# Kernel tuning notes

Hardware: AMD Instinct MI355X
Metric: run time of the kernel (lower is better)

The kernel has to match this reference:

```python
import jax, jax.numpy as jnp
import numpy as np

HEAD_SIZE = 64
INPUT_SIZE = 1024
B, T = 8, 2048


def setup_inputs() -> dict:
    key = jax.random.key(0)
    kx, kq, kk, kv = jax.random.split(key, 4)
    x = jax.random.normal(kx, (B, T, INPUT_SIZE), dtype=jnp.float32)
    s = 1.0 / np.sqrt(INPUT_SIZE)
    Wq = jax.random.uniform(kq, (INPUT_SIZE, HEAD_SIZE), minval=-s, maxval=s, dtype=jnp.float32)
    Wk = jax.random.uniform(kk, (INPUT_SIZE, HEAD_SIZE), minval=-s, maxval=s, dtype=jnp.float32)
    Wv = jax.random.uniform(kv, (INPUT_SIZE, HEAD_SIZE), minval=-s, maxval=s, dtype=jnp.float32)
    return {"x": x, "Wq": Wq, "Wk": Wk, "Wv": Wv}


def reference(x, Wq, Wk, Wv):
    # Faithful to the torch module: scores = K @ Q^T (note: keys times queries^T),
    # causal mask on upper triangle of that matrix, softmax over last axis,
    # dropout treated as identity (eval), then scores @ V.
    q = jnp.einsum('bti,ih->bth', x, Wq)  # [B,T,H]
    k = jnp.einsum('bti,ih->bth', x, Wk)
    v = jnp.einsum('bti,ih->bth', x, Wv)
    scale = HEAD_SIZE ** -0.5
    scores = jnp.einsum('bth,bsh->bts', k, q) * scale  # [B,T,T] = K Q^T
    Tlen = x.shape[1]
    causal = jnp.tril(jnp.ones((Tlen, Tlen), dtype=bool))
    scores = jnp.where(causal, scores, -jnp.inf)
    w = jax.nn.softmax(scores, axis=-1)
    out = jnp.einsum('bts,bsh->bth', w, v)  # [B,T,H]
    return out
```

## Files before the change

### kernel.cpp

```cpp
#include <hip/hip_runtime.h>

typedef __bf16 bf16_t;
typedef bf16_t bf16x8 __attribute__((ext_vector_type(8)));
typedef float f32x4 __attribute__((ext_vector_type(4)));

#define NB 8
#define TT 2048
#define DIN 1024
#define HH 64
#define MM (NB * TT)

__device__ __forceinline__ unsigned short f2bf(float f) {
    unsigned int u = __float_as_uint(f);
    u += 0x7fffu + ((u >> 16) & 1u);
    return (unsigned short)(u >> 16);
}

__device__ __forceinline__ int block_detect_f32(const unsigned int* __restrict__ xw,
                                                int tid, int* sflag) {
    if (tid < 64) {
        unsigned int u = xw[tid];
        unsigned int e = (u >> 7) & 0xFFu;
        unsigned long long m = __ballot(e >= 100u && e <= 150u);
        if (tid == 0) *sflag = (__popcll(m) < 48) ? 1 : 0;
    }
    __syncthreads();
    return *sflag;
}

__global__ __launch_bounds__(256) void transpose_w_kernel(
    const void* __restrict__ Wq, const void* __restrict__ Wk,
    const void* __restrict__ Wv, const unsigned int* __restrict__ xw,
    unsigned short* __restrict__ Wt) {
    __shared__ int sflag;
    __shared__ unsigned short ts[64][68];
    const int tid = threadIdx.x;
    const int isf32 = block_detect_f32(xw, tid, &sflag);
    const int w = blockIdx.x >> 4, kt = blockIdx.x & 15;
    const void* W = (w == 0) ? Wq : (w == 1) ? Wk : Wv;
    const int kk = tid >> 4, nn = (tid & 15) * 4;
#pragma unroll
    for (int j = 0; j < 4; ++j) {
        int k = kk + j * 16;
        if (isf32) {
            float4 f = *(const float4*)((const float*)W + (size_t)(kt * 64 + k) * 64 + nn);
            ts[k][nn + 0] = f2bf(f.x); ts[k][nn + 1] = f2bf(f.y);
            ts[k][nn + 2] = f2bf(f.z); ts[k][nn + 3] = f2bf(f.w);
        } else {
            *(uint2*)&ts[k][nn] =
                *(const uint2*)((const unsigned short*)W + (size_t)(kt * 64 + k) * 64 + nn);
        }
    }
    __syncthreads();
    const int n = tid >> 2, k0 = (tid & 3) * 16;
    unsigned short tmp[16];
#pragma unroll
    for (int j = 0; j < 16; ++j) tmp[j] = ts[k0 + j][n];
    unsigned short* dst = Wt + (size_t)(w * 64 + n) * 1024 + kt * 64 + k0;
    *(uint4*)(dst + 0) = *(uint4*)&tmp[0];
    *(uint4*)(dst + 8) = *(uint4*)&tmp[8];
}

__global__ __launch_bounds__(256) void proj_kernel(
    const void* __restrict__ xraw, const unsigned short* __restrict__ Wt,
    unsigned short* __restrict__ qbuf, unsigned short* __restrict__ kbuf,
    unsigned short* __restrict__ vtbuf) {
    __shared__ int sflag;
    __shared__ __align__(16) unsigned short xs[32][72];
    __shared__ __align__(16) unsigned short wts[192][72];

    const int tid = threadIdx.x;
    const int isf32 = block_detect_f32((const unsigned int*)xraw, tid, &sflag);
    const int m0 = blockIdx.x * 32;
    const int wave = tid >> 6, lane = tid & 63, quad = lane >> 4, l15 = lane & 15;
    const int rw = wave & 1, cw = wave >> 1;

    f32x4 acc[6];
#pragma unroll
    for (int c = 0; c < 6; ++c) acc[c] = (f32x4){0.f, 0.f, 0.f, 0.f};

    const float* xf = (const float*)xraw;
    const unsigned short* xb = (const unsigned short*)xraw;
    const int xr = tid >> 3, xc = (tid & 7) * 8;

    for (int k0 = 0; k0 < DIN; k0 += 64) {
        if (isf32) {
            const float* gp = xf + (size_t)(m0 + xr) * DIN + k0 + xc;
            float4 f0 = *(const float4*)(gp + 0);
            float4 f1 = *(const float4*)(gp + 4);
            unsigned short t[8] = {f2bf(f0.x), f2bf(f0.y), f2bf(f0.z), f2bf(f0.w),
                                   f2bf(f1.x), f2bf(f1.y), f2bf(f1.z), f2bf(f1.w)};
            *(uint4*)&xs[xr][xc] = *(uint4*)t;
        } else {
            *(uint4*)&xs[xr][xc] =
                *(const uint4*)(xb + (size_t)(m0 + xr) * DIN + k0 + xc);
        }
#pragma unroll
        for (int j = 0; j < 6; ++j) {
            int u = tid + j * 256;
            int n = u >> 3, cc = (u & 7) * 8;
            *(uint4*)&wts[n][cc] = *(const uint4*)(Wt + (size_t)n * 1024 + k0 + cc);
        }
        __syncthreads();
#pragma unroll
        for (int ks = 0; ks < 2; ++ks) {
            bf16x8 a = *(const bf16x8*)&xs[rw * 16 + l15][ks * 32 + quad * 8];
#pragma unroll
            for (int c = 0; c < 6; ++c) {
                bf16x8 bb = *(const bf16x8*)&wts[(cw * 6 + c) * 16 + l15][ks * 32 + quad * 8];
                acc[c] = __builtin_amdgcn_mfma_f32_16x16x32_bf16(a, bb, acc[c], 0, 0, 0);
            }
        }
        __syncthreads();
    }

#pragma unroll
    for (int c = 0; c < 6; ++c) {
        int cg = cw * 6 + c;
        int wsel = cg >> 2;
        int nn = (cg & 3) * 16 + l15;
#pragma unroll
        for (int reg = 0; reg < 4; ++reg) {
            int m = m0 + rw * 16 + quad * 4 + reg;
            unsigned short bv = f2bf(acc[c][reg]);
            if (wsel == 0)      qbuf[(size_t)m * HH + nn] = bv;
            else if (wsel == 1) kbuf[(size_t)m * HH + nn] = bv;
            else {
                int bb = m >> 11, t = m & 2047;
                vtbuf[((size_t)bb * HH + nn) * TT + t] = bv;
            }
        }
    }
}

__global__ __launch_bounds__(256) void attn_kernel(
    const unsigned short* __restrict__ rowbuf,
    const unsigned short* __restrict__ colbuf,
    const unsigned short* __restrict__ vtbuf,
    float* __restrict__ O_part,
    float* __restrict__ l_part) {

    __shared__ __align__(16) unsigned short Qr_s[64][72];
    __shared__ __align__(16) unsigned short Kc_s[64][72];
    __shared__ __align__(16) unsigned short Vt_s[64][72];
    __shared__ __align__(16) unsigned short P_s[4][16][72];

    const int tid  = threadIdx.x;
    const int bx   = blockIdx.x;
    const int b    = blockIdx.y;
    int rt, ch;
    if (bx < 8)       { rt = bx;                 ch = 0; }
    else if (bx < 24) { rt = 8 + ((bx - 8) >> 1);  ch = (bx - 8) & 1; }
    else if (bx < 48) { rt = 16 + (bx - 24) / 3;   ch = (bx - 24) % 3; }
    else              { rt = 24 + ((bx - 48) >> 2); ch = (bx - 48) & 3; }
    const int nct = min(8, rt + 1 - ch * 8);
    const int t0 = rt * 64;
    const int slot = b * 80 + bx;

    const int wave = tid >> 6, lane = tid & 63, quad = lane >> 4, l15 = lane & 15;
    const int sr = tid >> 2, sc = (tid & 3) * 16;

    {
        const uint4* g = (const uint4*)(rowbuf + ((size_t)b * TT + t0 + sr) * HH + sc);
        *(uint4*)&Qr_s[sr][sc + 0] = g[0];
        *(uint4*)&Qr_s[sr][sc + 8] = g[1];
    }

    f32x4 o[4];
#pragma unroll
    for (int c = 0; c < 4; ++c) o[c] = (f32x4){0.f, 0.f, 0.f, 0.f};
    float ls[4] = {0.f, 0.f, 0.f, 0.f};

    const float SCL2 = 0.125f * 1.4426950408889634f;

    for (int i = 0; i < nct; ++i) {
        const int stc = ch * 8 + i;
        const int s0 = stc * 64;
        {
            const uint4* gk = (const uint4*)(colbuf + ((size_t)b * TT + s0 + sr) * HH + sc);
            uint4 k0 = gk[0], k1 = gk[1];
            const uint4* gv = (const uint4*)(vtbuf + ((size_t)b * HH + sr) * TT + s0 + sc);
            uint4 v0 = gv[0], v1 = gv[1];
            *(uint4*)&Kc_s[sr][sc + 0] = k0;
            *(uint4*)&Kc_s[sr][sc + 8] = k1;
            *(uint4*)&Vt_s[sr][sc + 0] = v0;
            *(uint4*)&Vt_s[sr][sc + 8] = v1;
        }
        __syncthreads();

        f32x4 scf[4];
#pragma unroll
        for (int c = 0; c < 4; ++c) scf[c] = (f32x4){0.f, 0.f, 0.f, 0.f};
#pragma unroll
        for (int ks = 0; ks < 2; ++ks) {
            bf16x8 a = *(const bf16x8*)&Qr_s[wave * 16 + l15][ks * 32 + quad * 8];
#pragma unroll
            for (int c = 0; c < 4; ++c) {
                bf16x8 bb = *(const bf16x8*)&Kc_s[c * 16 + l15][ks * 32 + quad * 8];
                scf[c] = __builtin_amdgcn_mfma_f32_16x16x32_bf16(a, bb, scf[c], 0, 0, 0);
            }
        }

        const bool diag = (stc == rt);
#pragma unroll
        for (int r = 0; r < 4; ++r) {
            const int tg = t0 + wave * 16 + quad * 4 + r;
#pragma unroll
            for (int c = 0; c < 4; ++c) {
                float arg = fmaf(scf[c][r], SCL2, -30.f);
                if (diag && (s0 + c * 16 + l15) > tg) arg = -200.f;
                float p = __builtin_amdgcn_exp2f(arg);
                P_s[wave][quad * 4 + r][c * 16 + l15] = f2bf(p);
                ls[r] += p;
            }
        }
#pragma unroll
        for (int ks = 0; ks < 2; ++ks) {
            bf16x8 ap = *(const bf16x8*)&P_s[wave][l15][ks * 32 + quad * 8];
#pragma unroll
            for (int c = 0; c < 4; ++c) {
                bf16x8 bv = *(const bf16x8*)&Vt_s[c * 16 + l15][ks * 32 + quad * 8];
                o[c] = __builtin_amdgcn_mfma_f32_16x16x32_bf16(ap, bv, o[c], 0, 0, 0);
            }
        }
        __syncthreads();
    }

#pragma unroll
    for (int r = 0; r < 4; ++r) {
#pragma unroll
        for (int off = 1; off < 16; off <<= 1) ls[r] += __shfl_xor(ls[r], off);
    }
    if (l15 == 0) {
#pragma unroll
        for (int r = 0; r < 4; ++r)
            l_part[(size_t)slot * 64 + wave * 16 + quad * 4 + r] = ls[r];
    }
#pragma unroll
    for (int c = 0; c < 4; ++c)
#pragma unroll
        for (int r = 0; r < 4; ++r)
            O_part[(size_t)slot * 4096 + (wave * 16 + quad * 4 + r) * 64 + c * 16 + l15] = o[c][r];
}

__global__ __launch_bounds__(256) void combine_kernel(
    const float* __restrict__ O_part, const float* __restrict__ l_part,
    const unsigned int* __restrict__ xw, void* __restrict__ outraw) {
    __shared__ int sflag;
    const int tid = threadIdx.x;
    const int isf32 = block_detect_f32(xw, tid, &sflag);
    const int rt = blockIdx.x, b = blockIdx.y;
    const int nch = rt / 8 + 1;
    const int off = (rt < 8) ? rt : (rt < 16) ? 8 + 2 * (rt - 8)
                   : (rt < 24) ? 24 + 3 * (rt - 16) : 48 + 4 * (rt - 24);
    const int slot0 = b * 80 + off;

    const int row = tid >> 2, cb = (tid & 3) * 16;
    f32x4 a[4];
#pragma unroll
    for (int q = 0; q < 4; ++q) a[q] = (f32x4){0.f, 0.f, 0.f, 0.f};
    float l = 0.f;
    for (int j = 0; j < nch; ++j) {
        const f32x4* p = (const f32x4*)(O_part + (size_t)(slot0 + j) * 4096 + row * 64 + cb);
#pragma unroll
        for (int q = 0; q < 4; ++q) a[q] += p[q];
        l += l_part[(size_t)(slot0 + j) * 64 + row];
    }
    const float inv = 1.f / l;
    const size_t base = ((size_t)b * TT + rt * 64 + row) * HH + cb;
    if (isf32) {
        float* outf = (float*)outraw;
#pragma unroll
        for (int q = 0; q < 4; ++q) {
            f32x4 v = a[q] * inv;
            *(f32x4*)(outf + base + q * 4) = v;
        }
    } else {
        unsigned short h[16];
#pragma unroll
        for (int q = 0; q < 4; ++q)
#pragma unroll
            for (int e = 0; e < 4; ++e) h[q * 4 + e] = f2bf(a[q][e] * inv);
        unsigned short* outb = (unsigned short*)outraw;
        *(uint4*)(outb + base + 0) = *(uint4*)&h[0];
        *(uint4*)(outb + base + 8) = *(uint4*)&h[8];
    }
}

extern "C" void kernel_launch(void* const* d_in, const int* in_sizes, int n_in,
                              void* d_out, int out_size, void* d_ws, size_t ws_size,
                              hipStream_t stream) {
    const void* x  = d_in[0];
    const void* Wq = d_in[1];
    const void* Wk = d_in[2];
    const void* Wv = d_in[3];
    unsigned short* ws = (unsigned short*)d_ws;

    unsigned short* qbuf  = ws;
    unsigned short* kbuf  = ws + (size_t)MM * HH;
    unsigned short* vtbuf = ws + (size_t)2 * MM * HH;
    unsigned short* wtbuf = ws + (size_t)3 * MM * HH;
    float* O_part = (float*)(ws + (size_t)3 * MM * HH + 3 * 65536);
    float* l_part = O_part + (size_t)640 * 4096;

    hipLaunchKernelGGL(transpose_w_kernel, dim3(48), dim3(256), 0, stream,
                       Wq, Wk, Wv, (const unsigned int*)x, wtbuf);
    hipLaunchKernelGGL(proj_kernel, dim3(512), dim3(256), 0, stream,
                       x, wtbuf, qbuf, kbuf, vtbuf);
    hipLaunchKernelGGL(attn_kernel, dim3(80, 8), dim3(256), 0, stream,
                       kbuf, qbuf, vtbuf, O_part, l_part);
    hipLaunchKernelGGL(combine_kernel, dim3(32, 8), dim3(256), 0, stream,
                       O_part, l_part, (const unsigned int*)x, d_out);
}
```

Before: 160.3 us.

## Double the projection row tile and prefetch next K-slice into registers

The projection kernel now processes 64 rows per block instead of 32, giving each wave a 2x6 MFMA tile so each loaded weight fragment is reused across two row tiles, and halves the grid to 256 blocks. Global loads for the next K slice are issued into registers before the current slice's MFMAs, overlapping memory latency with compute. This raises register pressure and halves the number of blocks, which may reduce occupancy and CU coverage on a large-CU device.

```diff
diff --git a/kernel.cpp b/kernel.cpp
--- a/kernel.cpp
+++ b/kernel.cpp
@@ -66,71 +66,112 @@
     unsigned short* __restrict__ qbuf, unsigned short* __restrict__ kbuf,
     unsigned short* __restrict__ vtbuf) {
     __shared__ int sflag;
-    __shared__ __align__(16) unsigned short xs[32][72];
+    __shared__ __align__(16) unsigned short xs[64][72];
     __shared__ __align__(16) unsigned short wts[192][72];
 
     const int tid = threadIdx.x;
     const int isf32 = block_detect_f32((const unsigned int*)xraw, tid, &sflag);
-    const int m0 = blockIdx.x * 32;
+    const int m0 = blockIdx.x * 64;
     const int wave = tid >> 6, lane = tid & 63, quad = lane >> 4, l15 = lane & 15;
     const int rw = wave & 1, cw = wave >> 1;
 
-    f32x4 acc[6];
-#pragma unroll
-    for (int c = 0; c < 6; ++c) acc[c] = (f32x4){0.f, 0.f, 0.f, 0.f};
+    f32x4 acc[2][6];
+#pragma unroll
+    for (int rt = 0; rt < 2; ++rt)
+#pragma unroll
+        for (int ct = 0; ct < 6; ++ct)
+            acc[rt][ct] = (f32x4){0.f, 0.f, 0.f, 0.f};
 
     const float* xf = (const float*)xraw;
     const unsigned short* xb = (const unsigned short*)xraw;
-    const int xr = tid >> 3, xc = (tid & 7) * 8;
-
-    for (int k0 = 0; k0 < DIN; k0 += 64) {
+
+    const int xrow = tid >> 2, xkb = (tid & 3) * 16;
+
+    float4 px[4];
+    uint4  pxb[2];
+    uint4  pw[6];
+
+    auto prefetch = [&](int k0) {
         if (isf32) {
-            const float* gp = xf + (size_t)(m0 + xr) * DIN + k0 + xc;
-            float4 f0 = *(const float4*)(gp + 0);
-            float4 f1 = *(const float4*)(gp + 4);
-            unsigned short t[8] = {f2bf(f0.x), f2bf(f0.y), f2bf(f0.z), f2bf(f0.w),
-                                   f2bf(f1.x), f2bf(f1.y), f2bf(f1.z), f2bf(f1.w)};
-            *(uint4*)&xs[xr][xc] = *(uint4*)t;
+            const float* gp = xf + (size_t)(m0 + xrow) * DIN + k0 + xkb;
+#pragma unroll
+            for (int j = 0; j < 4; ++j) px[j] = *(const float4*)(gp + j * 4);
         } else {
-            *(uint4*)&xs[xr][xc] =
-                *(const uint4*)(xb + (size_t)(m0 + xr) * DIN + k0 + xc);
+            const unsigned short* gp = xb + (size_t)(m0 + xrow) * DIN + k0 + xkb;
+            pxb[0] = *(const uint4*)(gp + 0);
+            pxb[1] = *(const uint4*)(gp + 8);
         }
 #pragma unroll
         for (int j = 0; j < 6; ++j) {
-            int u = tid + j * 256;
-            int n = u >> 3, cc = (u & 7) * 8;
-            *(uint4*)&wts[n][cc] = *(const uint4*)(Wt + (size_t)n * 1024 + k0 + cc);
-        }
+            int c = tid + j * 256;
+            int row = c >> 3, kc = c & 7;
+            pw[j] = *(const uint4*)(Wt + (size_t)row * 1024 + k0 + kc * 8);
+        }
+    };
+
+    prefetch(0);
+
+    for (int it = 0; it < 16; ++it) {
         __syncthreads();
+        if (isf32) {
+            unsigned short t[16];
+#pragma unroll
+            for (int j = 0; j < 4; ++j) {
+                t[j * 4 + 0] = f2bf(px[j].x); t[j * 4 + 1] = f2bf(px[j].y);
+                t[j * 4 + 2] = f2bf(px[j].z); t[j * 4 + 3] = f2bf(px[j].w);
+            }
+            *(uint4*)&xs[xrow][xkb + 0] = *(uint4*)&t[0];
+            *(uint4*)&xs[xrow][xkb + 8] = *(uint4*)&t[8];
+        } else {
+            *(uint4*)&xs[xrow][xkb + 0] = pxb[0];
+            *(uint4*)&xs[xrow][xkb + 8] = pxb[1];
+        }
+#pragma unroll
+        for (int j = 0; j < 6; ++j) {
+            int c = tid + j * 256;
+            int row = c >> 3, kc = c & 7;
+            *(uint4*)&wts[row][kc * 8] = pw[j];
+        }
+        __syncthreads();
+
+        if (it < 15) prefetch((it + 1) * 64);
+
 #pragma unroll
         for (int ks = 0; ks < 2; ++ks) {
-            bf16x8 a = *(const bf16x8*)&xs[rw * 16 + l15][ks * 32 + quad * 8];
-#pragma unroll
-            for (int c = 0; c < 6; ++c) {
-                bf16x8 bb = *(const bf16x8*)&wts[(cw * 6 + c) * 16 + l15][ks * 32 + quad * 8];
-                acc[c] = __builtin_amdgcn_mfma_f32_16x16x32_bf16(a, bb, acc[c], 0, 0, 0);
-            }
-        }
-        __syncthreads();
-    }
-
-#pragma unroll
-    for (int c = 0; c < 6; ++c) {
-        int cg = cw * 6 + c;
-        int wsel = cg >> 2;
-        int nn = (cg & 3) * 16 + l15;
-#pragma unroll
-        for (int reg = 0; reg < 4; ++reg) {
-            int m = m0 + rw * 16 + quad * 4 + reg;
-            unsigned short bv = f2bf(acc[c][reg]);
-            if (wsel == 0)      qbuf[(size_t)m * HH + nn] = bv;
-            else if (wsel == 1) kbuf[(size_t)m * HH + nn] = bv;
-            else {
-                int bb = m >> 11, t = m & 2047;
-                vtbuf[((size_t)bb * HH + nn) * TT + t] = bv;
-            }
-        }
-    }
+            bf16x8 a[2], b[6];
+#pragma unroll
+            for (int rt = 0; rt < 2; ++rt)
+                a[rt] = *(const bf16x8*)&xs[rw * 32 + rt * 16 + l15][ks * 32 + quad * 8];
+#pragma unroll
+            for (int ct = 0; ct < 6; ++ct)
+                b[ct] = *(const bf16x8*)&wts[cw * 96 + ct * 16 + l15][ks * 32 + quad * 8];
+#pragma unroll
+            for (int rt = 0; rt < 2; ++rt)
+#pragma unroll
+                for (int ct = 0; ct < 6; ++ct)
+                    acc[rt][ct] = __builtin_amdgcn_mfma_f32_16x16x32_bf16(
+                        a[rt], b[ct], acc[rt][ct], 0, 0, 0);
+        }
+    }
+
+#pragma unroll
+    for (int rt = 0; rt < 2; ++rt)
+#pragma unroll
+        for (int ct = 0; ct < 6; ++ct) {
+            int n = cw * 96 + ct * 16 + l15;
+            int wsel = n >> 6, nn = n & 63;
+#pragma unroll
+            for (int reg = 0; reg < 4; ++reg) {
+                int m = m0 + rw * 32 + rt * 16 + quad * 4 + reg;
+                unsigned short bv = f2bf(acc[rt][ct][reg]);
+                if (wsel == 0)      qbuf[(size_t)m * HH + nn] = bv;
+                else if (wsel == 1) kbuf[(size_t)m * HH + nn] = bv;
+                else {
+                    int bb = m >> 11, t = m & 2047;
+                    vtbuf[((size_t)bb * HH + nn) * TT + t] = bv;
+                }
+            }
+        }
 }
 
 __global__ __launch_bounds__(256) void attn_kernel(
@@ -305,7 +346,7 @@
 
     hipLaunchKernelGGL(transpose_w_kernel, dim3(48), dim3(256), 0, stream,
                        Wq, Wk, Wv, (const unsigned int*)x, wtbuf);
-    hipLaunchKernelGGL(proj_kernel, dim3(512), dim3(256), 0, stream,
+    hipLaunchKernelGGL(proj_kernel, dim3(256), dim3(256), 0, stream,
                        x, wtbuf, qbuf, kbuf, vtbuf);
     hipLaunchKernelGGL(attn_kernel, dim3(80, 8), dim3(256), 0, stream,
                        kbuf, qbuf, vtbuf, O_part, l_part);
```

Result: no change. 159.6 us (-0.4%).

## Load projection operands directly into registers with double-buffered prefetch

Applied to the files above, without the earlier changes.

The projection kernel no longer stages x and W tiles through shared memory with two barriers per k-step. Each lane now loads its MFMA operand fragments straight from global memory into registers, prefetching the next 64-wide chunk while the current one computes, and the loop is fully unrolled. Launch bounds now request two blocks per CU. This removes LDS traffic and synchronisation but raises register pressure, and global loads become less coalesced because each lane reads 16-byte pieces from a different row.

```diff
diff --git a/kernel.cpp b/kernel.cpp
--- a/kernel.cpp
+++ b/kernel.cpp
@@ -61,68 +61,86 @@
     *(uint4*)(dst + 8) = *(uint4*)&tmp[8];
 }
 
-__global__ __launch_bounds__(256) void proj_kernel(
+__global__ __launch_bounds__(256, 2) void proj_kernel(
     const void* __restrict__ xraw, const unsigned short* __restrict__ Wt,
     unsigned short* __restrict__ qbuf, unsigned short* __restrict__ kbuf,
     unsigned short* __restrict__ vtbuf) {
     __shared__ int sflag;
-    __shared__ __align__(16) unsigned short xs[32][72];
-    __shared__ __align__(16) unsigned short wts[192][72];
-
     const int tid = threadIdx.x;
     const int isf32 = block_detect_f32((const unsigned int*)xraw, tid, &sflag);
     const int m0 = blockIdx.x * 32;
     const int wave = tid >> 6, lane = tid & 63, quad = lane >> 4, l15 = lane & 15;
     const int rw = wave & 1, cw = wave >> 1;
 
-    f32x4 acc[6];
-#pragma unroll
-    for (int c = 0; c < 6; ++c) acc[c] = (f32x4){0.f, 0.f, 0.f, 0.f};
-
     const float* xf = (const float*)xraw;
     const unsigned short* xb = (const unsigned short*)xraw;
-    const int xr = tid >> 3, xc = (tid & 7) * 8;
-
-    for (int k0 = 0; k0 < DIN; k0 += 64) {
+    const size_t arow = (size_t)(m0 + rw * 16 + l15) * DIN;
+    const unsigned short* wrow = Wt + (size_t)(cw * 96 + l15) * 1024;
+
+    f32x4 acc[6];
+#pragma unroll
+    for (int ct = 0; ct < 6; ++ct) acc[ct] = (f32x4){0.f, 0.f, 0.f, 0.f};
+
+    float4 pa[2][4];
+    uint4  pab[2][2];
+    uint4  pb[2][12];
+
+    auto load_chunk = [&](int buf, int k0) {
         if (isf32) {
-            const float* gp = xf + (size_t)(m0 + xr) * DIN + k0 + xc;
-            float4 f0 = *(const float4*)(gp + 0);
-            float4 f1 = *(const float4*)(gp + 4);
-            unsigned short t[8] = {f2bf(f0.x), f2bf(f0.y), f2bf(f0.z), f2bf(f0.w),
-                                   f2bf(f1.x), f2bf(f1.y), f2bf(f1.z), f2bf(f1.w)};
-            *(uint4*)&xs[xr][xc] = *(uint4*)t;
+#pragma unroll
+            for (int ks = 0; ks < 2; ++ks)
+#pragma unroll
+                for (int h = 0; h < 2; ++h)
+                    pa[buf][ks * 2 + h] =
+                        *(const float4*)(xf + arow + k0 + ks * 32 + quad * 8 + h * 4);
         } else {
-            *(uint4*)&xs[xr][xc] =
-                *(const uint4*)(xb + (size_t)(m0 + xr) * DIN + k0 + xc);
-        }
-#pragma unroll
-        for (int j = 0; j < 6; ++j) {
-            int u = tid + j * 256;
-            int n = u >> 3, cc = (u & 7) * 8;
-            *(uint4*)&wts[n][cc] = *(const uint4*)(Wt + (size_t)n * 1024 + k0 + cc);
-        }
-        __syncthreads();
+#pragma unroll
+            for (int ks = 0; ks < 2; ++ks)
+                pab[buf][ks] = *(const uint4*)(xb + arow + k0 + ks * 32 + quad * 8);
+        }
+#pragma unroll
+        for (int ks = 0; ks < 2; ++ks)
+#pragma unroll
+            for (int ct = 0; ct < 6; ++ct)
+                pb[buf][ks * 6 + ct] =
+                    *(const uint4*)(wrow + (size_t)ct * 16384 + k0 + ks * 32 + quad * 8);
+    };
+
+    auto compute_chunk = [&](int buf) {
 #pragma unroll
         for (int ks = 0; ks < 2; ++ks) {
-            bf16x8 a = *(const bf16x8*)&xs[rw * 16 + l15][ks * 32 + quad * 8];
-#pragma unroll
-            for (int c = 0; c < 6; ++c) {
-                bf16x8 bb = *(const bf16x8*)&wts[(cw * 6 + c) * 16 + l15][ks * 32 + quad * 8];
-                acc[c] = __builtin_amdgcn_mfma_f32_16x16x32_bf16(a, bb, acc[c], 0, 0, 0);
-            }
-        }
-        __syncthreads();
-    }
-
-#pragma unroll
-    for (int c = 0; c < 6; ++c) {
-        int cg = cw * 6 + c;
-        int wsel = cg >> 2;
-        int nn = (cg & 3) * 16 + l15;
+            bf16x8 a;
+            if (isf32) {
+                float4 f0 = pa[buf][ks * 2], f1 = pa[buf][ks * 2 + 1];
+                unsigned short t[8] = {f2bf(f0.x), f2bf(f0.y), f2bf(f0.z), f2bf(f0.w),
+                                       f2bf(f1.x), f2bf(f1.y), f2bf(f1.z), f2bf(f1.w)};
+                a = *(bf16x8*)t;
+            } else {
+                a = *(bf16x8*)&pab[buf][ks];
+            }
+#pragma unroll
+            for (int ct = 0; ct < 6; ++ct)
+                acc[ct] = __builtin_amdgcn_mfma_f32_16x16x32_bf16(
+                    a, *(bf16x8*)&pb[buf][ks * 6 + ct], acc[ct], 0, 0, 0);
+        }
+    };
+
+    load_chunk(0, 0);
+#pragma unroll
+    for (int it = 0; it < 16; ++it) {
+        const int cur = it & 1;
+        if (it < 15) load_chunk(cur ^ 1, (it + 1) * 64);
+        compute_chunk(cur);
+    }
+
+#pragma unroll
+    for (int ct = 0; ct < 6; ++ct) {
+        int n = cw * 96 + ct * 16 + l15;
+        int wsel = n >> 6, nn = n & 63;
 #pragma unroll
         for (int reg = 0; reg < 4; ++reg) {
             int m = m0 + rw * 16 + quad * 4 + reg;
-            unsigned short bv = f2bf(acc[c][reg]);
+            unsigned short bv = f2bf(acc[ct][reg]);
             if (wsel == 0)      qbuf[(size_t)m * HH + nn] = bv;
             else if (wsel == 1) kbuf[(size_t)m * HH + nn] = bv;
             else {
```

After: 171.3 us. +6.9%, slower.
